# Kernel tuning notes

Hardware: AMD Instinct MI355X
Metric: run time of the kernel (lower is better)

## Reference

```python
import jax, jax.numpy as jnp
import numpy as np

EPS = 1e-12

def _normalize(v):
    n = jnp.linalg.norm(v, axis=-1, keepdims=True)
    return v / jnp.maximum(n, EPS)

def _bgs(J):
    # J: [b, N, D, 3, 2] -> rotation matrices R [b, N, D, 3, 3]
    b1 = _normalize(J[..., :, 0])
    a2 = J[..., :, 1]
    dot = jnp.sum(b1 * a2, axis=-1, keepdims=True)
    b2 = _normalize(a2 - dot * b1)
    b3 = jnp.cross(b1, b2)
    return jnp.stack([b1, b2, b3], axis=-1)  # columns b1,b2,b3

def setup_inputs() -> dict:
    key = jax.random.key(0)
    k1, k2, k3, k4, k5 = jax.random.split(key, 5)
    B, N, D, OUT = 16, 4096, 64, 64
    X = jax.random.normal(k1, (B, N, D, 3), dtype=jnp.float32)
    J = jax.random.normal(k2, (B, N, D, 3, 2), dtype=jnp.float32)
    A = jax.random.normal(k3, (OUT, D), dtype=jnp.float32)
    Bm = jax.random.normal(k4, (OUT, D), dtype=jnp.float32)
    C = jax.random.normal(k5, (OUT, D), dtype=jnp.float32)
    return {"X": X, "J": J, "A": A, "Bm": Bm, "C": C}

def reference(X, J, A, Bm, C):
    R = _bgs(J)  # [b, N, D, 3, 3]
    # RT_i . X == column i of R dotted with X -> scalar per channel
    RTX = jnp.einsum('bndij,bndi->bndj', R, X)  # [b, N, D, 3], j-th entry = RT_j X
    rt0 = RTX[..., 0:1]
    rt1 = RTX[..., 1:2]
    rt2 = RTX[..., 2:3]
    col0 = R[..., :, 0]
    col1 = R[..., :, 1]
    col2 = R[..., :, 2]
    # a_term (after adding b_term, as in original forward)
    a_term = col1 * rt1 + col2 * rt2 + col2 * rt1 - col1 * rt2  # [b, N, D, 3]
    c_term = col0 * rt0
    Y = jnp.einsum('fe,bnei->bnfi', A, a_term) + jnp.einsum('fe,bnei->bnfi', C, c_term)
    Y = jnp.einsum('fe,bnei->bnfi', Bm, Y)
    return Y
```

## Files before the change

### kernel.cpp

```cpp
#include <hip/hip_runtime.h>


typedef __bf16 bf16x8 __attribute__((ext_vector_type(8)));
typedef float floatx4 __attribute__((ext_vector_type(4)));

#define RS 136

__global__ __launch_bounds__(256) void prep_kernel(const float* __restrict__ A,
                                                   const float* __restrict__ Bm,
                                                   const float* __restrict__ C,
                                                   __bf16* __restrict__ acat) {
    int tid = blockIdx.x * 256 + threadIdx.x;
    int f = tid >> 6;
    int e = tid & 63;
    float m = 0.f, m2 = 0.f;
    #pragma unroll 8
    for (int k = 0; k < 64; ++k) {
        float b = Bm[f * 64 + k];
        m  = fmaf(b, A[k * 64 + e], m);
        m2 = fmaf(b, C[k * 64 + e], m2);
    }
    acat[f * 128 + e]      = (__bf16)m;
    acat[f * 128 + 64 + e] = (__bf16)m2;
}

__global__ __launch_bounds__(256, 3) void main_kernel(const float* __restrict__ X,
                                                      const float* __restrict__ J,
                                                      const __bf16* __restrict__ acat,
                                                      float* __restrict__ out) {
    __shared__ __align__(16) float buf[4][3328];

    const int wave = threadIdx.x >> 6;
    const int lane = threadIdx.x & 63;
    const int l15  = lane & 15;
    const int quad = lane >> 4;
    const int pbase = blockIdx.x * 64 + wave * 16;

    bf16x8 afrag[4][4];
    #pragma unroll
    for (int mt = 0; mt < 4; ++mt)
        #pragma unroll
        for (int kc = 0; kc < 4; ++kc)
            afrag[mt][kc] = *(const bf16x8*)(acat + (mt * 16 + l15) * 128 + kc * 32 + quad * 8);

    __bf16* zw = (__bf16*)buf[wave];

    #pragma unroll 2
    for (int pi = 0; pi < 16; ++pi) {
        const size_t p = (size_t)(pbase + pi);
        const float2* jp = (const float2*)(J + p * 384) + lane * 3;
        float2 ja = jp[0], jb = jp[1], jc = jp[2];
        const float* xp = X + p * 192 + lane * 3;
        float xx = xp[0], xy = xp[1], xz = xp[2];

        float a0x = ja.x, a0y = jb.x, a0z = jc.x;
        float a1x = ja.y, a1y = jb.y, a1z = jc.y;

        float n0 = sqrtf(a0x * a0x + a0y * a0y + a0z * a0z);
        float r0 = 1.0f / fmaxf(n0, 1e-12f);
        float b1x = a0x * r0, b1y = a0y * r0, b1z = a0z * r0;

        float d  = b1x * a1x + b1y * a1y + b1z * a1z;
        float ux = a1x - d * b1x, uy = a1y - d * b1y, uz = a1z - d * b1z;
        float n2 = sqrtf(ux * ux + uy * uy + uz * uz);
        float r2 = 1.0f / fmaxf(n2, 1e-12f);
        float b2x = ux * r2, b2y = uy * r2, b2z = uz * r2;

        float b3x = b1y * b2z - b1z * b2y;
        float b3y = b1z * b2x - b1x * b2z;
        float b3z = b1x * b2y - b1y * b2x;

        float rt0 = b1x * xx + b1y * xy + b1z * xz;
        float rt1 = b2x * xx + b2y * xy + b2z * xz;
        float rt2 = b3x * xx + b3y * xy + b3z * xz;

        float s = rt1 - rt2, t = rt1 + rt2;

        __bf16* zr = zw + (pi * 3) * RS;
        zr[lane]               = (__bf16)(b2x * s + b3x * t);
        zr[64 + lane]          = (__bf16)(b1x * rt0);
        zr[RS + lane]          = (__bf16)(b2y * s + b3y * t);
        zr[RS + 64 + lane]     = (__bf16)(b1y * rt0);
        zr[2 * RS + lane]      = (__bf16)(b2z * s + b3z * t);
        zr[2 * RS + 64 + lane] = (__bf16)(b1z * rt0);
    }

    __asm__ volatile("s_waitcnt lgkmcnt(0)" ::: "memory");

    floatx4 acc[4][3];
    #pragma unroll
    for (int mt = 0; mt < 4; ++mt)
        #pragma unroll
        for (int nt = 0; nt < 3; ++nt)
            acc[mt][nt] = (floatx4){0.f, 0.f, 0.f, 0.f};

    #pragma unroll
    for (int kc = 0; kc < 4; ++kc) {
        #pragma unroll
        for (int nt = 0; nt < 3; ++nt) {
            bf16x8 b = *(const bf16x8*)(zw + (nt * 16 + l15) * RS + kc * 32 + quad * 8);
            #pragma unroll
            for (int mt = 0; mt < 4; ++mt)
                acc[mt][nt] = __builtin_amdgcn_mfma_f32_16x16x32_bf16(
                    afrag[mt][kc], b, acc[mt][nt], 0, 0, 0);
        }
    }

    __asm__ volatile("s_waitcnt lgkmcnt(0)" ::: "memory");

    float* dl = buf[wave];
    #pragma unroll
    for (int mt = 0; mt < 4; ++mt) {
        #pragma unroll
        for (int nt = 0; nt < 3; ++nt) {
            int n  = nt * 16 + l15;
            int pl = (n * 21846) >> 16;
            int i  = n - pl * 3;
            float* dst = dl + pl * 192 + i;
            #pragma unroll
            for (int r = 0; r < 4; ++r) {
                int f = mt * 16 + quad * 4 + r;
                dst[f * 3] = acc[mt][nt][r];
            }
        }
    }

    __asm__ volatile("s_waitcnt lgkmcnt(0)" ::: "memory");

    const floatx4* s4 = (const floatx4*)dl;
    floatx4* og = (floatx4*)(out + (size_t)pbase * 192);
    #pragma unroll
    for (int t = 0; t < 12; ++t)
        og[t * 64 + lane] = s4[t * 64 + lane];
}

extern "C" void kernel_launch(void* const* d_in, const int* in_sizes, int n_in,
                              void* d_out, int out_size, void* d_ws, size_t ws_size,
                              hipStream_t stream) {
    const float* X  = (const float*)d_in[0];
    const float* J  = (const float*)d_in[1];
    const float* A  = (const float*)d_in[2];
    const float* Bm = (const float*)d_in[3];
    const float* C  = (const float*)d_in[4];
    float* out = (float*)d_out;
    __bf16* acat = (__bf16*)d_ws;

    prep_kernel<<<16, 256, 0, stream>>>(A, Bm, C, acat);

    main_kernel<<<1024, 256, 0, stream>>>(X, J, acat, out);
}
```

Baseline: 212.6 us.

## Halve points per wave, interleave K layout, and raise occupancy

```diff
diff --git a/kernel.cpp b/kernel.cpp
--- a/kernel.cpp
+++ b/kernel.cpp
@@ -4,7 +4,7 @@
 typedef __bf16 bf16x8 __attribute__((ext_vector_type(8)));
 typedef float floatx4 __attribute__((ext_vector_type(4)));
 
-#define RS 136
+#define RSW 68
 
 __global__ __launch_bounds__(256) void prep_kernel(const float* __restrict__ A,
                                                    const float* __restrict__ Bm,
@@ -20,33 +20,32 @@
         m  = fmaf(b, A[k * 64 + e], m);
         m2 = fmaf(b, C[k * 64 + e], m2);
     }
-    acat[f * 128 + e]      = (__bf16)m;
-    acat[f * 128 + 64 + e] = (__bf16)m2;
+    acat[f * 128 + 2 * e]     = (__bf16)m;
+    acat[f * 128 + 2 * e + 1] = (__bf16)m2;
 }
 
-__global__ __launch_bounds__(256, 3) void main_kernel(const float* __restrict__ X,
+static __device__ __forceinline__ unsigned pk(float a, float c) {
+    unsigned short ua = __builtin_bit_cast(unsigned short, (__bf16)a);
+    unsigned short uc = __builtin_bit_cast(unsigned short, (__bf16)c);
+    return ((unsigned)uc << 16) | ua;
+}
+
+__global__ __launch_bounds__(256, 5) void main_kernel(const float* __restrict__ X,
                                                       const float* __restrict__ J,
                                                       const __bf16* __restrict__ acat,
                                                       float* __restrict__ out) {
-    __shared__ __align__(16) float buf[4][3328];
+    __shared__ __align__(16) float buf[4][1632];
 
     const int wave = threadIdx.x >> 6;
     const int lane = threadIdx.x & 63;
     const int l15  = lane & 15;
     const int quad = lane >> 4;
-    const int pbase = blockIdx.x * 64 + wave * 16;
+    const int pbase = blockIdx.x * 32 + wave * 8;
 
-    bf16x8 afrag[4][4];
-    #pragma unroll
-    for (int mt = 0; mt < 4; ++mt)
-        #pragma unroll
-        for (int kc = 0; kc < 4; ++kc)
-            afrag[mt][kc] = *(const bf16x8*)(acat + (mt * 16 + l15) * 128 + kc * 32 + quad * 8);
+    unsigned* zw = (unsigned*)buf[wave];
 
-    __bf16* zw = (__bf16*)buf[wave];
-
-    #pragma unroll 2
-    for (int pi = 0; pi < 16; ++pi) {
+    #pragma unroll 4
+    for (int pi = 0; pi < 8; ++pi) {
         const size_t p = (size_t)(pbase + pi);
         const float2* jp = (const float2*)(J + p * 384) + lane * 3;
         float2 ja = jp[0], jb = jp[1], jc = jp[2];
@@ -76,29 +75,35 @@
 
         float s = rt1 - rt2, t = rt1 + rt2;
 
-        __bf16* zr = zw + (pi * 3) * RS;
-        zr[lane]               = (__bf16)(b2x * s + b3x * t);
-        zr[64 + lane]          = (__bf16)(b1x * rt0);
-        zr[RS + lane]          = (__bf16)(b2y * s + b3y * t);
-        zr[RS + 64 + lane]     = (__bf16)(b1y * rt0);
-        zr[2 * RS + lane]      = (__bf16)(b2z * s + b3z * t);
-        zr[2 * RS + 64 + lane] = (__bf16)(b1z * rt0);
+        unsigned* zr = zw + (pi * 3) * RSW;
+        zr[lane]           = pk(b2x * s + b3x * t, b1x * rt0);
+        zr[RSW + lane]     = pk(b2y * s + b3y * t, b1y * rt0);
+        zr[2 * RSW + lane] = pk(b2z * s + b3z * t, b1z * rt0);
     }
+
+    bf16x8 afrag[4][4];
+    #pragma unroll
+    for (int mt = 0; mt < 4; ++mt)
+        #pragma unroll
+        for (int kc = 0; kc < 4; ++kc)
+            afrag[mt][kc] = *(const bf16x8*)(acat + (mt * 16 + l15) * 128 + kc * 32 + quad * 8);
 
     __asm__ volatile("s_waitcnt lgkmcnt(0)" ::: "memory");
 
-    floatx4 acc[4][3];
+    floatx4 acc[4][2];
     #pragma unroll
     for (int mt = 0; mt < 4; ++mt)
         #pragma unroll
-        for (int nt = 0; nt < 3; ++nt)
+        for (int nt = 0; nt < 2; ++nt)
             acc[mt][nt] = (floatx4){0.f, 0.f, 0.f, 0.f};
 
     #pragma unroll
     for (int kc = 0; kc < 4; ++kc) {
         #pragma unroll
-        for (int nt = 0; nt < 3; ++nt) {
-            bf16x8 b = *(const bf16x8*)(zw + (nt * 16 + l15) * RS + kc * 32 + quad * 8);
+        for (int nt = 0; nt < 2; ++nt) {
+            int row = nt * 16 + l15;
+            row = row > 23 ? 23 : row;
+            bf16x8 b = *(const bf16x8*)((const __bf16*)zw + row * 136 + kc * 32 + quad * 8);
             #pragma unroll
             for (int mt = 0; mt < 4; ++mt)
                 acc[mt][nt] = __builtin_amdgcn_mfma_f32_16x16x32_bf16(
@@ -112,26 +117,31 @@
     #pragma unroll
     for (int mt = 0; mt < 4; ++mt) {
         #pragma unroll
-        for (int nt = 0; nt < 3; ++nt) {
-            int n  = nt * 16 + l15;
-            int pl = (n * 21846) >> 16;
-            int i  = n - pl * 3;
-            float* dst = dl + pl * 192 + i;
-            #pragma unroll
-            for (int r = 0; r < 4; ++r) {
-                int f = mt * 16 + quad * 4 + r;
-                dst[f * 3] = acc[mt][nt][r];
+        for (int nt = 0; nt < 2; ++nt) {
+            int n = nt * 16 + l15;
+            if (n < 24) {
+                int pl = (n * 21846) >> 16;
+                int i  = n - pl * 3;
+                float* dst = dl + pl * 196 + i;
+                #pragma unroll
+                for (int r = 0; r < 4; ++r) {
+                    int f = mt * 16 + quad * 4 + r;
+                    dst[f * 3] = acc[mt][nt][r];
+                }
             }
         }
     }
 
     __asm__ volatile("s_waitcnt lgkmcnt(0)" ::: "memory");
 
-    const floatx4* s4 = (const floatx4*)dl;
     floatx4* og = (floatx4*)(out + (size_t)pbase * 192);
     #pragma unroll
-    for (int t = 0; t < 12; ++t)
-        og[t * 64 + lane] = s4[t * 64 + lane];
+    for (int t = 0; t < 6; ++t) {
+        int g  = t * 64 + lane;
+        int pg = (g * 1366) >> 16;
+        int o  = g - pg * 48;
+        og[g] = *(const floatx4*)(dl + pg * 196 + o * 4);
+    }
 }
 
 extern "C" void kernel_launch(void* const* d_in, const int* in_sizes, int n_in,
@@ -147,5 +157,5 @@
 
     prep_kernel<<<16, 256, 0, stream>>>(A, Bm, C, acat);
 
-    main_kernel<<<1024, 256, 0, stream>>>(X, J, acat, out);
+    main_kernel<<<2048, 256, 0, stream>>>(X, J, acat, out);
 }
```

Result: slower. 219.8 us (+3.4%).
